# Kernel tuning notes

Measured on AMD Instinct MI355X. Metric: run time of the kernel, lower is better.

The kernel has to match this reference:

```python
import jax, jax.numpy as jnp
import numpy as np

N = 50000      # nodes
E = 800000     # edges
P = 200000     # link pairs
D_IN = 128     # input_dim
F_NUM = 128    # filter_num
OUT = 2        # out_dim
K = 10         # APPNP propagation steps
ALPHA = 0.1    # teleport prob


def setup_inputs() -> dict:
    key = jax.random.key(0)
    ks = jax.random.split(key, 9)
    x = jax.random.normal(ks[0], (N, D_IN), dtype=jnp.float32)
    edge_index = jax.random.randint(ks[1], (2, E), 0, N)
    index = jax.random.randint(ks[2], (P, 2), 0, N)
    s1 = 1.0 / np.sqrt(D_IN)
    s2 = 1.0 / np.sqrt(F_NUM)
    s3 = 1.0 / np.sqrt(2 * F_NUM)
    W1 = jax.random.uniform(ks[3], (F_NUM, D_IN), minval=-s1, maxval=s1)
    b1 = jax.random.uniform(ks[4], (F_NUM,), minval=-s1, maxval=s1)
    W2 = jax.random.uniform(ks[5], (F_NUM, F_NUM), minval=-s2, maxval=s2)
    b2 = jax.random.uniform(ks[6], (F_NUM,), minval=-s2, maxval=s2)
    W3 = jax.random.uniform(ks[7], (OUT, 2 * F_NUM), minval=-s3, maxval=s3)
    b3 = jax.random.uniform(ks[8], (OUT,), minval=-s3, maxval=s3)
    return {"x": x, "edge_index": edge_index, "index": index,
            "W1": W1, "b1": b1, "W2": W2, "b2": b2, "W3": W3, "b3": b3}


def _gcn_norm(edge_index, num_nodes):
    # PyG gcn_norm: add self-loops, sym norm D^{-1/2} (A+I) D^{-1/2}
    src, dst = edge_index[0], edge_index[1]
    loop = jnp.arange(num_nodes, dtype=src.dtype)
    src = jnp.concatenate([src, loop])
    dst = jnp.concatenate([dst, loop])
    deg = jax.ops.segment_sum(jnp.ones_like(src, dtype=jnp.float32), dst,
                              num_segments=num_nodes)
    dinv = jnp.where(deg > 0, jax.lax.rsqrt(deg), 0.0)
    norm = dinv[src] * dinv[dst]  # [E+N]
    return src, dst, norm


def _appnp(x, src, dst, norm, num_nodes):
    # h_{k+1} = (1-alpha) * A_hat h_k + alpha * x0
    def step(h, _):
        agg = jax.ops.segment_sum(norm[:, None] * h[src], dst,
                                  num_segments=num_nodes)
        return (1.0 - ALPHA) * agg + ALPHA * x, None
    h, _ = jax.lax.scan(step, x, None, length=K)
    return h


def reference(x, edge_index, index, W1, b1, W2, b2, W3, b3):
    num_nodes = x.shape[0]
    src, dst, norm = _gcn_norm(edge_index, num_nodes)
    h = x @ W1.T + b1                      # [N, F]
    h = jax.nn.relu(_appnp(h, src, dst, norm, num_nodes))
    h = h @ W2.T + b2                      # [N, F]
    h = jax.nn.relu(_appnp(h, src, dst, norm, num_nodes))
    feat = jnp.concatenate([h[index[:, 0]], h[index[:, 1]]], axis=-1)  # [P, 2F]
    out = feat @ W3.T + b3                 # [P, OUT]
    return jax.nn.log_softmax(out, axis=1)
```

## Files before the change

### kernel.cpp

```cpp
#include <hip/hip_runtime.h>
#include <math.h>

#define NN 50000
#define NE 800000
#define NP 200000
#define NF 128
#define NEDGE_TOT (NE + NN)
#define NBLK 196

typedef __attribute__((ext_vector_type(8))) short short8;
typedef __attribute__((ext_vector_type(4))) float float4v;

__device__ __forceinline__ float bf_lo(unsigned u) { return __uint_as_float(u << 16); }
__device__ __forceinline__ float bf_hi(unsigned u) { return __uint_as_float(u & 0xffff0000u); }
__device__ __forceinline__ unsigned short f2bf(float f) {
    unsigned u = __float_as_uint(f);
    return (unsigned short)((u + 0x7fffu + ((u >> 16) & 1u)) >> 16);
}
__device__ __forceinline__ unsigned pack2bf(float a, float b) {
    return (unsigned)f2bf(a) | ((unsigned)f2bf(b) << 16);
}

__global__ __launch_bounds__(256) void init_cnt_k(int* __restrict__ cnt) {
    int i = blockIdx.x * 256 + threadIdx.x;
    if (i < NN) cnt[i] = 1;
}

__global__ __launch_bounds__(256) void count_k(const int* __restrict__ ei,
                                               int* __restrict__ cnt) {
    int e = blockIdx.x * 256 + threadIdx.x;
    if (e < NE) atomicAdd(&cnt[ei[NE + e]], 1);
}

__global__ __launch_bounds__(256) void scan_reduce_k(const int* __restrict__ cnt,
                                                     int* __restrict__ bsum,
                                                     float* __restrict__ dinv) {
    __shared__ int s[256];
    int t = threadIdx.x;
    int idx = blockIdx.x * 256 + t;
    int v = (idx < NN) ? cnt[idx] : 0;
    if (idx < NN) dinv[idx] = rsqrtf((float)v);
    s[t] = v;
    __syncthreads();
    for (int off = 128; off > 0; off >>= 1) {
        if (t < off) s[t] += s[t + off];
        __syncthreads();
    }
    if (t == 0) bsum[blockIdx.x] = s[0];
}

__global__ __launch_bounds__(256) void scan_bsums_k(const int* __restrict__ bsum,
                                                    int* __restrict__ boff) {
    __shared__ int s[256];
    int t = threadIdx.x;
    int v = (t < NBLK) ? bsum[t] : 0;
    s[t] = v;
    __syncthreads();
    for (int off = 1; off < 256; off <<= 1) {
        int add = (t >= off) ? s[t - off] : 0;
        __syncthreads();
        s[t] += add;
        __syncthreads();
    }
    if (t < NBLK) boff[t] = s[t] - v;
}

__global__ __launch_bounds__(256) void scan_down_k(const int* __restrict__ cnt,
                                                   const int* __restrict__ boff,
                                                   int* __restrict__ row_ptr,
                                                   int* __restrict__ wptr) {
    __shared__ int s[256];
    int t = threadIdx.x;
    int idx = blockIdx.x * 256 + t;
    int v = (idx < NN) ? cnt[idx] : 0;
    s[t] = v;
    __syncthreads();
    for (int off = 1; off < 256; off <<= 1) {
        int add = (t >= off) ? s[t - off] : 0;
        __syncthreads();
        s[t] += add;
        __syncthreads();
    }
    int excl = s[t] - v + boff[blockIdx.x];
    if (idx < NN) {
        row_ptr[idx] = excl;
        wptr[idx] = excl;
        if (idx == NN - 1) row_ptr[NN] = excl + v;
    }
}

__global__ __launch_bounds__(256) void scatter_k(const int* __restrict__ ei,
                                                 const float* __restrict__ dinv,
                                                 int* __restrict__ wptr,
                                                 int* __restrict__ cols,
                                                 float* __restrict__ norms) {
    int e = blockIdx.x * 256 + threadIdx.x;
    if (e >= NEDGE_TOT) return;
    int s, d;
    if (e < NE) { s = ei[e]; d = ei[NE + e]; }
    else        { s = d = e - NE; }
    int pos = atomicAdd(&wptr[d], 1);
    cols[pos]  = s;
    norms[pos] = dinv[s] * dinv[d];
}

__global__ __launch_bounds__(256) void cast_x_k(const float* __restrict__ x,
                                                unsigned short* __restrict__ Xb) {
    int t = blockIdx.x * 256 + threadIdx.x;
    if (t >= NN * 16) return;
    int i = t * 8;
    float4 f0 = *(const float4*)(x + i);
    float4 f1 = *(const float4*)(x + i + 4);
    uint4 q;
    q.x = pack2bf(f0.x, f0.y);
    q.y = pack2bf(f0.z, f0.w);
    q.z = pack2bf(f1.x, f1.y);
    q.w = pack2bf(f1.z, f1.w);
    *(uint4*)(Xb + i) = q;
}

__global__ __launch_bounds__(256) void cast_w_k(const float* __restrict__ W,
                                                unsigned short* __restrict__ Wb) {
    int t = blockIdx.x * 256 + threadIdx.x;
    if (t >= 128 * 128 / 8) return;
    int i = t * 8;
    float4 f0 = *(const float4*)(W + i);
    float4 f1 = *(const float4*)(W + i + 4);
    uint4 q;
    q.x = pack2bf(f0.x, f0.y);
    q.y = pack2bf(f0.z, f0.w);
    q.z = pack2bf(f1.x, f1.y);
    q.w = pack2bf(f1.z, f1.w);
    *(uint4*)(Wb + i) = q;
}

#define GPAD 136
__global__ __launch_bounds__(256) void gemm_mfma_k(const unsigned short* __restrict__ Xb,
                                                   const unsigned short* __restrict__ Wb,
                                                   const float* __restrict__ bias,
                                                   unsigned short* __restrict__ Yb,
                                                   int nrows) {
    __shared__ unsigned short sm[4 * 16 * GPAD];
    int wave = threadIdx.x >> 6, lane = threadIdx.x & 63;
    int rbase = blockIdx.x * 64 + wave * 16;
    if (rbase >= nrows) return;
    int quad = lane >> 4, mn = lane & 15;
    float4v acc[8];
#pragma unroll
    for (int ft = 0; ft < 8; ++ft) acc[ft] = (float4v){0.f, 0.f, 0.f, 0.f};
#pragma unroll
    for (int kb = 0; kb < 128; kb += 32) {
        short8 a = *(const short8*)(Xb + (size_t)(rbase + mn) * NF + kb + quad * 8);
#pragma unroll
        for (int ft = 0; ft < 8; ++ft) {
            short8 b = *(const short8*)(Wb + (size_t)(ft * 16 + mn) * NF + kb + quad * 8);
            acc[ft] = __builtin_amdgcn_mfma_f32_16x16x32_bf16(a, b, acc[ft], 0, 0, 0);
        }
    }
    unsigned short* smw = sm + wave * 16 * GPAD;
#pragma unroll
    for (int ft = 0; ft < 8; ++ft) {
        float bv = bias[ft * 16 + mn];
#pragma unroll
        for (int r = 0; r < 4; ++r)
            smw[(quad * 4 + r) * GPAD + ft * 16 + mn] = f2bf(acc[ft][r] + bv);
    }
    __syncthreads();
#pragma unroll
    for (int t = 0; t < 4; ++t) {
        int rl = t * 4 + quad;
        uint4 q = *(const uint4*)(smw + rl * GPAD + mn * 8);
        *(uint4*)(Yb + (size_t)(rbase + rl) * NF + mn * 8) = q;
    }
}

__global__ __launch_bounds__(256) void appnp_bf16_k(const unsigned short* __restrict__ h,
                                                    const unsigned short* __restrict__ x0,
                                                    unsigned short* __restrict__ out,
                                                    const int* __restrict__ row_ptr,
                                                    const int* __restrict__ cols,
                                                    const float* __restrict__ norms,
                                                    int relu) {
    int wid = (blockIdx.x * 256 + threadIdx.x) >> 6;
    int lane = threadIdx.x & 63;
    if (wid >= NN) return;
    int half = lane >> 5, li = lane & 31;
    int beg = row_ptr[wid], end = row_ptr[wid + 1];
    float a0 = 0.f, a1 = 0.f, a2 = 0.f, a3 = 0.f;
    for (int e = beg; e < end; e += 64) {
        int m = end - e;
        if (m > 64) m = 64;
        int c = 0;
        float w = 0.f;
        if (lane < m) { c = cols[e + lane]; w = norms[e + lane]; }
        int j = 0;
        for (; j + 8 <= m; j += 8) {
#pragma unroll
            for (int p = 0; p < 4; ++p) {
                int src = j + 2 * p + half;
                int cj = __shfl(c, src, 64);
                float wj = __shfl(w, src, 64);
                uint2 q = *((const uint2*)(h + (size_t)cj * NF) + li);
                a0 += wj * bf_lo(q.x);
                a1 += wj * bf_hi(q.x);
                a2 += wj * bf_lo(q.y);
                a3 += wj * bf_hi(q.y);
            }
        }
        for (; j < m; j += 2) {
            int src = j + half;
            int cj = __shfl(c, src, 64);
            float wj = __shfl(w, src, 64);
            uint2 q = *((const uint2*)(h + (size_t)cj * NF) + li);
            a0 += wj * bf_lo(q.x);
            a1 += wj * bf_hi(q.x);
            a2 += wj * bf_lo(q.y);
            a3 += wj * bf_hi(q.y);
        }
    }
    a0 += __shfl_xor(a0, 32, 64);
    a1 += __shfl_xor(a1, 32, 64);
    a2 += __shfl_xor(a2, 32, 64);
    a3 += __shfl_xor(a3, 32, 64);
    if (half == 0) {
        uint2 xq = *((const uint2*)(x0 + (size_t)wid * NF) + li);
        float r0 = 0.9f * a0 + 0.1f * bf_lo(xq.x);
        float r1 = 0.9f * a1 + 0.1f * bf_hi(xq.x);
        float r2 = 0.9f * a2 + 0.1f * bf_lo(xq.y);
        float r3 = 0.9f * a3 + 0.1f * bf_hi(xq.y);
        if (relu) {
            r0 = fmaxf(r0, 0.f); r1 = fmaxf(r1, 0.f);
            r2 = fmaxf(r2, 0.f); r3 = fmaxf(r3, 0.f);
        }
        uint2 oq;
        oq.x = pack2bf(r0, r1);
        oq.y = pack2bf(r2, r3);
        *((uint2*)(out + (size_t)wid * NF) + li) = oq;
    }
}

__global__ __launch_bounds__(256) void pair_k(const unsigned short* __restrict__ h,
                                              const int* __restrict__ index,
                                              const float* __restrict__ W3,
                                              const float* __restrict__ b3,
                                              float* __restrict__ outp) {
    int gw = (blockIdx.x * 256 + threadIdx.x) >> 6;
    int lane = threadIdx.x & 63;
    if (gw >= NP) return;
    int half = lane >> 5, li = lane & 31;
    int u = index[gw * 2], v = index[gw * 2 + 1];
    int node = half ? v : u;
    uint2 q = *((const uint2*)(h + (size_t)node * NF) + li);
    float f0 = bf_lo(q.x), f1 = bf_hi(q.x), f2 = bf_lo(q.y), f3 = bf_hi(q.y);
    int fb = half * 128 + li * 4;
    float4 wa = *(const float4*)(W3 + fb);
    float4 wb = *(const float4*)(W3 + 256 + fb);
    float p0 = f0 * wa.x + f1 * wa.y + f2 * wa.z + f3 * wa.w;
    float p1 = f0 * wb.x + f1 * wb.y + f2 * wb.z + f3 * wb.w;
#pragma unroll
    for (int off = 32; off > 0; off >>= 1) {
        p0 += __shfl_xor(p0, off, 64);
        p1 += __shfl_xor(p1, off, 64);
    }
    if (lane == 0) {
        float s0 = p0 + b3[0], s1 = p1 + b3[1];
        float m = fmaxf(s0, s1);
        float lse = m + logf(expf(s0 - m) + expf(s1 - m));
        *(float2*)(outp + (size_t)gw * 2) = make_float2(s0 - lse, s1 - lse);
    }
}

extern "C" void kernel_launch(void* const* d_in, const int* in_sizes, int n_in,
                              void* d_out, int out_size, void* d_ws, size_t ws_size,
                              hipStream_t stream) {
    const float* x  = (const float*)d_in[0];
    const int* ei   = (const int*)d_in[1];
    const int* idx  = (const int*)d_in[2];
    const float* W1 = (const float*)d_in[3];
    const float* b1 = (const float*)d_in[4];
    const float* W2 = (const float*)d_in[5];
    const float* b2 = (const float*)d_in[6];
    const float* W3 = (const float*)d_in[7];
    const float* b3 = (const float*)d_in[8];
    float* out = (float*)d_out;

    char* ws = (char*)d_ws;
    size_t off = 0;
    auto alloc = [&](size_t bytes) -> void* {
        void* p = ws + off;
        off = (off + bytes + 255) & ~(size_t)255;
        return p;
    };
    int*   cnt     = (int*)  alloc(NN * sizeof(int));
    float* dinv    = (float*)alloc(NN * sizeof(float));
    int*   row_ptr = (int*)  alloc((NN + 1) * sizeof(int));
    int*   wptr    = (int*)  alloc(NN * sizeof(int));
    int*   bsum    = (int*)  alloc(NBLK * sizeof(int));
    int*   boff    = (int*)  alloc(NBLK * sizeof(int));
    int*   cols    = (int*)  alloc(NEDGE_TOT * sizeof(int));
    float* norms   = (float*)alloc(NEDGE_TOT * sizeof(float));
    unsigned short* Xb  = (unsigned short*)alloc((size_t)NN * NF * 2);
    unsigned short* Wb1 = (unsigned short*)alloc(128 * 128 * 2);
    unsigned short* Wb2 = (unsigned short*)alloc(128 * 128 * 2);
    unsigned short* H0  = (unsigned short*)alloc((size_t)NN * NF * 2);
    unsigned short* HA  = (unsigned short*)alloc((size_t)NN * NF * 2);
    unsigned short* HB  = (unsigned short*)alloc((size_t)NN * NF * 2);

    const int gN    = (NN + 255) / 256;
    const int gE    = (NE + 255) / 256;
    const int gET   = (NEDGE_TOT + 255) / 256;
    const int gGemm = (NN + 63) / 64;
    const int gStep = (NN * 64 + 255) / 256;
    const int gPair = (NP * 64 + 255) / 256;

    cast_w_k<<<8, 256, 0, stream>>>(W1, Wb1);
    cast_w_k<<<8, 256, 0, stream>>>(W2, Wb2);
    cast_x_k<<<(NN * 16 + 255) / 256, 256, 0, stream>>>(x, Xb);
    init_cnt_k<<<gN, 256, 0, stream>>>(cnt);
    count_k<<<gE, 256, 0, stream>>>(ei, cnt);
    scan_reduce_k<<<NBLK, 256, 0, stream>>>(cnt, bsum, dinv);
    scan_bsums_k<<<1, 256, 0, stream>>>(bsum, boff);
    scan_down_k<<<NBLK, 256, 0, stream>>>(cnt, boff, row_ptr, wptr);
    scatter_k<<<gET, 256, 0, stream>>>(ei, dinv, wptr, cols, norms);

    gemm_mfma_k<<<gGemm, 256, 0, stream>>>(Xb, Wb1, b1, H0, NN);
    {
        const unsigned short* cur = H0;
        for (int k = 0; k < 10; ++k) {
            unsigned short* dst = (k & 1) ? HB : HA;
            appnp_bf16_k<<<gStep, 256, 0, stream>>>(cur, H0, dst, row_ptr, cols,
                                                    norms, (k == 9) ? 1 : 0);
            cur = dst;
        }
    }
    gemm_mfma_k<<<gGemm, 256, 0, stream>>>(HB, Wb2, b2, H0, NN);
    {
        const unsigned short* cur = H0;
        for (int k = 0; k < 10; ++k) {
            unsigned short* dst = (k & 1) ? HB : HA;
            appnp_bf16_k<<<gStep, 256, 0, stream>>>(cur, H0, dst, row_ptr, cols,
                                                    norms, (k == 9) ? 1 : 0);
            cur = dst;
        }
    }
    pair_k<<<gPair, 256, 0, stream>>>(HB, idx, W3, b3, out);
}
```

Measured before the change: 919.3 us.

## Pack edge records, gather four neighbors per wave, precompute per-node link projections

Edge column and norm are interleaved into one int2 array so each edge needs a single load. The APPNP kernel now splits the wave into four 16-lane groups, each reading a full 256-byte row with uint4 loads. That processes four neighbors per iteration, with a cross-group shuffle reduction at the end. The last propagation step projects each node onto the W3 halves, so the pair kernel reads two float4 per pair instead of two full feature rows. This removes most of the per-pair gather traffic at the cost of more registers and a small change in summation order.

```diff
diff --git a/kernel.cpp b/kernel.cpp
--- a/kernel.cpp
+++ b/kernel.cpp
@@ -92,16 +92,17 @@
 __global__ __launch_bounds__(256) void scatter_k(const int* __restrict__ ei,
                                                  const float* __restrict__ dinv,
                                                  int* __restrict__ wptr,
-                                                 int* __restrict__ cols,
-                                                 float* __restrict__ norms) {
+                                                 int2* __restrict__ rec) {
     int e = blockIdx.x * 256 + threadIdx.x;
     if (e >= NEDGE_TOT) return;
     int s, d;
     if (e < NE) { s = ei[e]; d = ei[NE + e]; }
     else        { s = d = e - NE; }
     int pos = atomicAdd(&wptr[d], 1);
-    cols[pos]  = s;
-    norms[pos] = dinv[s] * dinv[d];
+    int2 r;
+    r.x = s;
+    r.y = __float_as_int(dinv[s] * dinv[d]);
+    rec[pos] = r;
 }
 
 __global__ __launch_bounds__(256) void cast_x_k(const float* __restrict__ x,
@@ -174,100 +175,122 @@
     }
 }
 
-__global__ __launch_bounds__(256) void appnp_bf16_k(const unsigned short* __restrict__ h,
-                                                    const unsigned short* __restrict__ x0,
-                                                    unsigned short* __restrict__ out,
-                                                    const int* __restrict__ row_ptr,
-                                                    const int* __restrict__ cols,
-                                                    const float* __restrict__ norms,
-                                                    int relu) {
+__global__ __launch_bounds__(256) void appnp4_k(const unsigned short* __restrict__ h,
+                                                const unsigned short* __restrict__ x0,
+                                                unsigned short* __restrict__ out,
+                                                const int* __restrict__ row_ptr,
+                                                const int2* __restrict__ rec,
+                                                int relu, int proj,
+                                                const float* __restrict__ W3,
+                                                float4* __restrict__ puv) {
     int wid = (blockIdx.x * 256 + threadIdx.x) >> 6;
     int lane = threadIdx.x & 63;
     if (wid >= NN) return;
-    int half = lane >> 5, li = lane & 31;
+    int g = lane >> 4, li = lane & 15;
     int beg = row_ptr[wid], end = row_ptr[wid + 1];
     float a0 = 0.f, a1 = 0.f, a2 = 0.f, a3 = 0.f;
+    float a4 = 0.f, a5 = 0.f, a6 = 0.f, a7 = 0.f;
     for (int e = beg; e < end; e += 64) {
         int m = end - e;
         if (m > 64) m = 64;
         int c = 0;
         float w = 0.f;
-        if (lane < m) { c = cols[e + lane]; w = norms[e + lane]; }
-        int j = 0;
-        for (; j + 8 <= m; j += 8) {
-#pragma unroll
-            for (int p = 0; p < 4; ++p) {
-                int src = j + 2 * p + half;
-                int cj = __shfl(c, src, 64);
-                float wj = __shfl(w, src, 64);
-                uint2 q = *((const uint2*)(h + (size_t)cj * NF) + li);
+        if (lane < m) { int2 q = rec[e + lane]; c = q.x; w = __int_as_float(q.y); }
+        for (int j = 0; j < m; j += 4) {
+            int src = j + g;
+            int cj = __shfl(c, src, 64);
+            float wj = __shfl(w, src, 64);
+            if (src < m) {
+                uint4 q = *((const uint4*)(h + (size_t)cj * NF) + li);
                 a0 += wj * bf_lo(q.x);
                 a1 += wj * bf_hi(q.x);
                 a2 += wj * bf_lo(q.y);
                 a3 += wj * bf_hi(q.y);
+                a4 += wj * bf_lo(q.z);
+                a5 += wj * bf_hi(q.z);
+                a6 += wj * bf_lo(q.w);
+                a7 += wj * bf_hi(q.w);
             }
         }
-        for (; j < m; j += 2) {
-            int src = j + half;
-            int cj = __shfl(c, src, 64);
-            float wj = __shfl(w, src, 64);
-            uint2 q = *((const uint2*)(h + (size_t)cj * NF) + li);
-            a0 += wj * bf_lo(q.x);
-            a1 += wj * bf_hi(q.x);
-            a2 += wj * bf_lo(q.y);
-            a3 += wj * bf_hi(q.y);
-        }
-    }
-    a0 += __shfl_xor(a0, 32, 64);
-    a1 += __shfl_xor(a1, 32, 64);
-    a2 += __shfl_xor(a2, 32, 64);
-    a3 += __shfl_xor(a3, 32, 64);
-    if (half == 0) {
-        uint2 xq = *((const uint2*)(x0 + (size_t)wid * NF) + li);
+    }
+#pragma unroll
+    for (int off = 16; off < 64; off <<= 1) {
+        a0 += __shfl_xor(a0, off, 64);
+        a1 += __shfl_xor(a1, off, 64);
+        a2 += __shfl_xor(a2, off, 64);
+        a3 += __shfl_xor(a3, off, 64);
+        a4 += __shfl_xor(a4, off, 64);
+        a5 += __shfl_xor(a5, off, 64);
+        a6 += __shfl_xor(a6, off, 64);
+        a7 += __shfl_xor(a7, off, 64);
+    }
+    if (g == 0) {
+        uint4 xq = *((const uint4*)(x0 + (size_t)wid * NF) + li);
         float r0 = 0.9f * a0 + 0.1f * bf_lo(xq.x);
         float r1 = 0.9f * a1 + 0.1f * bf_hi(xq.x);
         float r2 = 0.9f * a2 + 0.1f * bf_lo(xq.y);
         float r3 = 0.9f * a3 + 0.1f * bf_hi(xq.y);
+        float r4 = 0.9f * a4 + 0.1f * bf_lo(xq.z);
+        float r5 = 0.9f * a5 + 0.1f * bf_hi(xq.z);
+        float r6 = 0.9f * a6 + 0.1f * bf_lo(xq.w);
+        float r7 = 0.9f * a7 + 0.1f * bf_hi(xq.w);
         if (relu) {
             r0 = fmaxf(r0, 0.f); r1 = fmaxf(r1, 0.f);
             r2 = fmaxf(r2, 0.f); r3 = fmaxf(r3, 0.f);
-        }
-        uint2 oq;
-        oq.x = pack2bf(r0, r1);
-        oq.y = pack2bf(r2, r3);
-        *((uint2*)(out + (size_t)wid * NF) + li) = oq;
-    }
-}
-
-__global__ __launch_bounds__(256) void pair_k(const unsigned short* __restrict__ h,
-                                              const int* __restrict__ index,
-                                              const float* __restrict__ W3,
-                                              const float* __restrict__ b3,
-                                              float* __restrict__ outp) {
-    int gw = (blockIdx.x * 256 + threadIdx.x) >> 6;
-    int lane = threadIdx.x & 63;
-    if (gw >= NP) return;
-    int half = lane >> 5, li = lane & 31;
-    int u = index[gw * 2], v = index[gw * 2 + 1];
-    int node = half ? v : u;
-    uint2 q = *((const uint2*)(h + (size_t)node * NF) + li);
-    float f0 = bf_lo(q.x), f1 = bf_hi(q.x), f2 = bf_lo(q.y), f3 = bf_hi(q.y);
-    int fb = half * 128 + li * 4;
-    float4 wa = *(const float4*)(W3 + fb);
-    float4 wb = *(const float4*)(W3 + 256 + fb);
-    float p0 = f0 * wa.x + f1 * wa.y + f2 * wa.z + f3 * wa.w;
-    float p1 = f0 * wb.x + f1 * wb.y + f2 * wb.z + f3 * wb.w;
-#pragma unroll
-    for (int off = 32; off > 0; off >>= 1) {
-        p0 += __shfl_xor(p0, off, 64);
-        p1 += __shfl_xor(p1, off, 64);
-    }
-    if (lane == 0) {
-        float s0 = p0 + b3[0], s1 = p1 + b3[1];
-        float m = fmaxf(s0, s1);
-        float lse = m + logf(expf(s0 - m) + expf(s1 - m));
-        *(float2*)(outp + (size_t)gw * 2) = make_float2(s0 - lse, s1 - lse);
-    }
+            r4 = fmaxf(r4, 0.f); r5 = fmaxf(r5, 0.f);
+            r6 = fmaxf(r6, 0.f); r7 = fmaxf(r7, 0.f);
+        }
+        if (!proj) {
+            uint4 oq;
+            oq.x = pack2bf(r0, r1);
+            oq.y = pack2bf(r2, r3);
+            oq.z = pack2bf(r4, r5);
+            oq.w = pack2bf(r6, r7);
+            *((uint4*)(out + (size_t)wid * NF) + li) = oq;
+        } else {
+            int fb = li * 8;
+            float4 wu0a = *(const float4*)(W3 + fb);
+            float4 wu0b = *(const float4*)(W3 + fb + 4);
+            float4 wv0a = *(const float4*)(W3 + 128 + fb);
+            float4 wv0b = *(const float4*)(W3 + 128 + fb + 4);
+            float4 wu1a = *(const float4*)(W3 + 256 + fb);
+            float4 wu1b = *(const float4*)(W3 + 256 + fb + 4);
+            float4 wv1a = *(const float4*)(W3 + 384 + fb);
+            float4 wv1b = *(const float4*)(W3 + 384 + fb + 4);
+            float du0 = r0 * wu0a.x + r1 * wu0a.y + r2 * wu0a.z + r3 * wu0a.w
+                      + r4 * wu0b.x + r5 * wu0b.y + r6 * wu0b.z + r7 * wu0b.w;
+            float du1 = r0 * wu1a.x + r1 * wu1a.y + r2 * wu1a.z + r3 * wu1a.w
+                      + r4 * wu1b.x + r5 * wu1b.y + r6 * wu1b.z + r7 * wu1b.w;
+            float dv0 = r0 * wv0a.x + r1 * wv0a.y + r2 * wv0a.z + r3 * wv0a.w
+                      + r4 * wv0b.x + r5 * wv0b.y + r6 * wv0b.z + r7 * wv0b.w;
+            float dv1 = r0 * wv1a.x + r1 * wv1a.y + r2 * wv1a.z + r3 * wv1a.w
+                      + r4 * wv1b.x + r5 * wv1b.y + r6 * wv1b.z + r7 * wv1b.w;
+#pragma unroll
+            for (int off = 1; off < 16; off <<= 1) {
+                du0 += __shfl_xor(du0, off, 64);
+                du1 += __shfl_xor(du1, off, 64);
+                dv0 += __shfl_xor(dv0, off, 64);
+                dv1 += __shfl_xor(dv1, off, 64);
+            }
+            if (li == 0) puv[wid] = make_float4(du0, du1, dv0, dv1);
+        }
+    }
+}
+
+__global__ __launch_bounds__(256) void pair2_k(const float4* __restrict__ puv,
+                                               const int2* __restrict__ index,
+                                               const float* __restrict__ b3,
+                                               float* __restrict__ outp) {
+    int p = blockIdx.x * 256 + threadIdx.x;
+    if (p >= NP) return;
+    int2 uv = index[p];
+    float4 a = puv[uv.x];
+    float4 b = puv[uv.y];
+    float s0 = a.x + b.z + b3[0];
+    float s1 = a.y + b.w + b3[1];
+    float m = fmaxf(s0, s1);
+    float lse = m + logf(expf(s0 - m) + expf(s1 - m));
+    *(float2*)(outp + (size_t)p * 2) = make_float2(s0 - lse, s1 - lse);
 }
 
 extern "C" void kernel_launch(void* const* d_in, const int* in_sizes, int n_in,
@@ -297,8 +320,8 @@
     int*   wptr    = (int*)  alloc(NN * sizeof(int));
     int*   bsum    = (int*)  alloc(NBLK * sizeof(int));
     int*   boff    = (int*)  alloc(NBLK * sizeof(int));
-    int*   cols    = (int*)  alloc(NEDGE_TOT * sizeof(int));
-    float* norms   = (float*)alloc(NEDGE_TOT * sizeof(float));
+    int2*  rec     = (int2*) alloc((size_t)NEDGE_TOT * sizeof(int2));
+    float4* puv    = (float4*)alloc((size_t)NN * sizeof(float4));
     unsigned short* Xb  = (unsigned short*)alloc((size_t)NN * NF * 2);
     unsigned short* Wb1 = (unsigned short*)alloc(128 * 128 * 2);
     unsigned short* Wb2 = (unsigned short*)alloc(128 * 128 * 2);
@@ -311,7 +334,7 @@
     const int gET   = (NEDGE_TOT + 255) / 256;
     const int gGemm = (NN + 63) / 64;
     const int gStep = (NN * 64 + 255) / 256;
-    const int gPair = (NP * 64 + 255) / 256;
+    const int gPair = (NP + 255) / 256;
 
     cast_w_k<<<8, 256, 0, stream>>>(W1, Wb1);
     cast_w_k<<<8, 256, 0, stream>>>(W2, Wb2);
@@ -321,15 +344,15 @@
     scan_reduce_k<<<NBLK, 256, 0, stream>>>(cnt, bsum, dinv);
     scan_bsums_k<<<1, 256, 0, stream>>>(bsum, boff);
     scan_down_k<<<NBLK, 256, 0, stream>>>(cnt, boff, row_ptr, wptr);
-    scatter_k<<<gET, 256, 0, stream>>>(ei, dinv, wptr, cols, norms);
+    scatter_k<<<gET, 256, 0, stream>>>(ei, dinv, wptr, rec);
 
     gemm_mfma_k<<<gGemm, 256, 0, stream>>>(Xb, Wb1, b1, H0, NN);
     {
         const unsigned short* cur = H0;
         for (int k = 0; k < 10; ++k) {
             unsigned short* dst = (k & 1) ? HB : HA;
-            appnp_bf16_k<<<gStep, 256, 0, stream>>>(cur, H0, dst, row_ptr, cols,
-                                                    norms, (k == 9) ? 1 : 0);
+            appnp4_k<<<gStep, 256, 0, stream>>>(cur, H0, dst, row_ptr, rec,
+                                                (k == 9) ? 1 : 0, 0, W3, puv);
             cur = dst;
         }
     }
@@ -338,10 +361,11 @@
         const unsigned short* cur = H0;
         for (int k = 0; k < 10; ++k) {
             unsigned short* dst = (k & 1) ? HB : HA;
-            appnp_bf16_k<<<gStep, 256, 0, stream>>>(cur, H0, dst, row_ptr, cols,
-                                                    norms, (k == 9) ? 1 : 0);
+            appnp4_k<<<gStep, 256, 0, stream>>>(cur, H0, dst, row_ptr, rec,
+                                                (k == 9) ? 1 : 0,
+                                                (k == 9) ? 1 : 0, W3, puv);
             cur = dst;
         }
     }
-    pair_k<<<gPair, 256, 0, stream>>>(HB, idx, W3, b3, out);
-}
+    pair2_k<<<gPair, 256, 0, stream>>>(puv, (const int2*)idx, b3, out);
+}
```

Result: no change. 909.7 us (-1.0%).

## Factor GCN norm into pre-scaled features, fuse casts and final projection

Applied to the files above, without the earlier changes.

Stores the propagated features pre-multiplied by dinv, so each APPNP step is an unweighted gather-sum plus one per-node scale, and the per-edge norms array is removed. The fp32 input cast is folded into the first GEMM. The final W3 projection is pushed into the last propagation step as per-node scalars, so the pair kernel reads 16 bytes per node instead of full feature rows. A zeroed padding row replaces masked edge lanes, which allows four independent gathers per iteration. The cost is extra bf16 rounding of the scaled features and more workspace buffers.

```diff
diff --git a/kernel.cpp b/kernel.cpp
--- a/kernel.cpp
+++ b/kernel.cpp
@@ -90,33 +90,23 @@
 }
 
 __global__ __launch_bounds__(256) void scatter_k(const int* __restrict__ ei,
-                                                 const float* __restrict__ dinv,
                                                  int* __restrict__ wptr,
-                                                 int* __restrict__ cols,
-                                                 float* __restrict__ norms) {
+                                                 int* __restrict__ cols) {
     int e = blockIdx.x * 256 + threadIdx.x;
     if (e >= NEDGE_TOT) return;
     int s, d;
     if (e < NE) { s = ei[e]; d = ei[NE + e]; }
     else        { s = d = e - NE; }
     int pos = atomicAdd(&wptr[d], 1);
-    cols[pos]  = s;
-    norms[pos] = dinv[s] * dinv[d];
-}
-
-__global__ __launch_bounds__(256) void cast_x_k(const float* __restrict__ x,
-                                                unsigned short* __restrict__ Xb) {
-    int t = blockIdx.x * 256 + threadIdx.x;
-    if (t >= NN * 16) return;
-    int i = t * 8;
-    float4 f0 = *(const float4*)(x + i);
-    float4 f1 = *(const float4*)(x + i + 4);
-    uint4 q;
-    q.x = pack2bf(f0.x, f0.y);
-    q.y = pack2bf(f0.z, f0.w);
-    q.z = pack2bf(f1.x, f1.y);
-    q.w = pack2bf(f1.z, f1.w);
-    *(uint4*)(Xb + i) = q;
+    cols[pos] = s;
+}
+
+__global__ __launch_bounds__(256) void zero_k(unsigned short* Ys1, unsigned short* Ys2,
+                                              unsigned short* HA, unsigned short* HB) {
+    int t = threadIdx.x;
+    unsigned short* bufs[4] = {Ys1, Ys2, HA, HB};
+    unsigned short* b = bufs[t >> 6];
+    ((unsigned*)(b + (size_t)NN * NF))[t & 63] = 0u;
 }
 
 __global__ __launch_bounds__(256) void cast_w_k(const float* __restrict__ W,
@@ -135,10 +125,13 @@
 }
 
 #define GPAD 136
-__global__ __launch_bounds__(256) void gemm_mfma_k(const unsigned short* __restrict__ Xb,
+template <bool F32IN>
+__global__ __launch_bounds__(256) void gemm_mfma_k(const void* __restrict__ Xv,
                                                    const unsigned short* __restrict__ Wb,
                                                    const float* __restrict__ bias,
-                                                   unsigned short* __restrict__ Yb,
+                                                   const float* __restrict__ dinv,
+                                                   unsigned short* __restrict__ Yu,
+                                                   unsigned short* __restrict__ Ys,
                                                    int nrows) {
     __shared__ unsigned short sm[4 * 16 * GPAD];
     int wave = threadIdx.x >> 6, lane = threadIdx.x & 63;
@@ -150,7 +143,19 @@
     for (int ft = 0; ft < 8; ++ft) acc[ft] = (float4v){0.f, 0.f, 0.f, 0.f};
 #pragma unroll
     for (int kb = 0; kb < 128; kb += 32) {
-        short8 a = *(const short8*)(Xb + (size_t)(rbase + mn) * NF + kb + quad * 8);
+        short8 a;
+        if (F32IN) {
+            const float* X = (const float*)Xv;
+            float4 f0 = *(const float4*)(X + (size_t)(rbase + mn) * NF + kb + quad * 8);
+            float4 f1 = *(const float4*)(X + (size_t)(rbase + mn) * NF + kb + quad * 8 + 4);
+            a[0] = (short)f2bf(f0.x); a[1] = (short)f2bf(f0.y);
+            a[2] = (short)f2bf(f0.z); a[3] = (short)f2bf(f0.w);
+            a[4] = (short)f2bf(f1.x); a[5] = (short)f2bf(f1.y);
+            a[6] = (short)f2bf(f1.z); a[7] = (short)f2bf(f1.w);
+        } else {
+            const unsigned short* X = (const unsigned short*)Xv;
+            a = *(const short8*)(X + (size_t)(rbase + mn) * NF + kb + quad * 8);
+        }
 #pragma unroll
         for (int ft = 0; ft < 8; ++ft) {
             short8 b = *(const short8*)(Wb + (size_t)(ft * 16 + mn) * NF + kb + quad * 8);
@@ -169,18 +174,28 @@
 #pragma unroll
     for (int t = 0; t < 4; ++t) {
         int rl = t * 4 + quad;
+        int row = rbase + rl;
         uint4 q = *(const uint4*)(smw + rl * GPAD + mn * 8);
-        *(uint4*)(Yb + (size_t)(rbase + rl) * NF + mn * 8) = q;
-    }
-}
-
-__global__ __launch_bounds__(256) void appnp_bf16_k(const unsigned short* __restrict__ h,
-                                                    const unsigned short* __restrict__ x0,
-                                                    unsigned short* __restrict__ out,
-                                                    const int* __restrict__ row_ptr,
-                                                    const int* __restrict__ cols,
-                                                    const float* __restrict__ norms,
-                                                    int relu) {
+        *(uint4*)(Yu + (size_t)row * NF + mn * 8) = q;
+        float g = dinv[row];
+        uint4 qs;
+        qs.x = pack2bf(g * bf_lo(q.x), g * bf_hi(q.x));
+        qs.y = pack2bf(g * bf_lo(q.y), g * bf_hi(q.y));
+        qs.z = pack2bf(g * bf_lo(q.z), g * bf_hi(q.z));
+        qs.w = pack2bf(g * bf_lo(q.w), g * bf_hi(q.w));
+        *(uint4*)(Ys + (size_t)row * NF + mn * 8) = qs;
+    }
+}
+
+__global__ __launch_bounds__(256) void appnp_s_k(const unsigned short* __restrict__ hs,
+                                                 const unsigned short* __restrict__ x0,
+                                                 const float* __restrict__ dinv,
+                                                 unsigned short* __restrict__ out,
+                                                 const int* __restrict__ row_ptr,
+                                                 const int* __restrict__ cols,
+                                                 int mode,
+                                                 const float* __restrict__ W3,
+                                                 float4* __restrict__ puv) {
     int wid = (blockIdx.x * 256 + threadIdx.x) >> 6;
     int lane = threadIdx.x & 63;
     if (wid >= NN) return;
@@ -190,32 +205,29 @@
     for (int e = beg; e < end; e += 64) {
         int m = end - e;
         if (m > 64) m = 64;
-        int c = 0;
-        float w = 0.f;
-        if (lane < m) { c = cols[e + lane]; w = norms[e + lane]; }
+        int c = (lane < m) ? cols[e + lane] : NN;
         int j = 0;
         for (; j + 8 <= m; j += 8) {
-#pragma unroll
-            for (int p = 0; p < 4; ++p) {
-                int src = j + 2 * p + half;
-                int cj = __shfl(c, src, 64);
-                float wj = __shfl(w, src, 64);
-                uint2 q = *((const uint2*)(h + (size_t)cj * NF) + li);
-                a0 += wj * bf_lo(q.x);
-                a1 += wj * bf_hi(q.x);
-                a2 += wj * bf_lo(q.y);
-                a3 += wj * bf_hi(q.y);
-            }
+            int c0 = __shfl(c, j + half, 64);
+            int c1 = __shfl(c, j + 2 + half, 64);
+            int c2 = __shfl(c, j + 4 + half, 64);
+            int c3 = __shfl(c, j + 6 + half, 64);
+            uint2 q0 = *((const uint2*)(hs + (size_t)c0 * NF) + li);
+            uint2 q1 = *((const uint2*)(hs + (size_t)c1 * NF) + li);
+            uint2 q2 = *((const uint2*)(hs + (size_t)c2 * NF) + li);
+            uint2 q3 = *((const uint2*)(hs + (size_t)c3 * NF) + li);
+            a0 += (bf_lo(q0.x) + bf_lo(q1.x)) + (bf_lo(q2.x) + bf_lo(q3.x));
+            a1 += (bf_hi(q0.x) + bf_hi(q1.x)) + (bf_hi(q2.x) + bf_hi(q3.x));
+            a2 += (bf_lo(q0.y) + bf_lo(q1.y)) + (bf_lo(q2.y) + bf_lo(q3.y));
+            a3 += (bf_hi(q0.y) + bf_hi(q1.y)) + (bf_hi(q2.y) + bf_hi(q3.y));
         }
         for (; j < m; j += 2) {
-            int src = j + half;
-            int cj = __shfl(c, src, 64);
-            float wj = __shfl(w, src, 64);
-            uint2 q = *((const uint2*)(h + (size_t)cj * NF) + li);
-            a0 += wj * bf_lo(q.x);
-            a1 += wj * bf_hi(q.x);
-            a2 += wj * bf_lo(q.y);
-            a3 += wj * bf_hi(q.y);
+            int cj = __shfl(c, j + half, 64);
+            uint2 q = *((const uint2*)(hs + (size_t)cj * NF) + li);
+            a0 += bf_lo(q.x);
+            a1 += bf_hi(q.x);
+            a2 += bf_lo(q.y);
+            a3 += bf_hi(q.y);
         }
     }
     a0 += __shfl_xor(a0, 32, 64);
@@ -223,51 +235,63 @@
     a2 += __shfl_xor(a2, 32, 64);
     a3 += __shfl_xor(a3, 32, 64);
     if (half == 0) {
+        float g = dinv[wid];
+        float s9 = 0.9f * g;
         uint2 xq = *((const uint2*)(x0 + (size_t)wid * NF) + li);
-        float r0 = 0.9f * a0 + 0.1f * bf_lo(xq.x);
-        float r1 = 0.9f * a1 + 0.1f * bf_hi(xq.x);
-        float r2 = 0.9f * a2 + 0.1f * bf_lo(xq.y);
-        float r3 = 0.9f * a3 + 0.1f * bf_hi(xq.y);
-        if (relu) {
-            r0 = fmaxf(r0, 0.f); r1 = fmaxf(r1, 0.f);
-            r2 = fmaxf(r2, 0.f); r3 = fmaxf(r3, 0.f);
-        }
-        uint2 oq;
-        oq.x = pack2bf(r0, r1);
-        oq.y = pack2bf(r2, r3);
-        *((uint2*)(out + (size_t)wid * NF) + li) = oq;
-    }
-}
-
-__global__ __launch_bounds__(256) void pair_k(const unsigned short* __restrict__ h,
-                                              const int* __restrict__ index,
-                                              const float* __restrict__ W3,
-                                              const float* __restrict__ b3,
-                                              float* __restrict__ outp) {
-    int gw = (blockIdx.x * 256 + threadIdx.x) >> 6;
-    int lane = threadIdx.x & 63;
-    if (gw >= NP) return;
-    int half = lane >> 5, li = lane & 31;
-    int u = index[gw * 2], v = index[gw * 2 + 1];
-    int node = half ? v : u;
-    uint2 q = *((const uint2*)(h + (size_t)node * NF) + li);
-    float f0 = bf_lo(q.x), f1 = bf_hi(q.x), f2 = bf_lo(q.y), f3 = bf_hi(q.y);
-    int fb = half * 128 + li * 4;
-    float4 wa = *(const float4*)(W3 + fb);
-    float4 wb = *(const float4*)(W3 + 256 + fb);
-    float p0 = f0 * wa.x + f1 * wa.y + f2 * wa.z + f3 * wa.w;
-    float p1 = f0 * wb.x + f1 * wb.y + f2 * wb.z + f3 * wb.w;
-#pragma unroll
-    for (int off = 32; off > 0; off >>= 1) {
-        p0 += __shfl_xor(p0, off, 64);
-        p1 += __shfl_xor(p1, off, 64);
-    }
-    if (lane == 0) {
-        float s0 = p0 + b3[0], s1 = p1 + b3[1];
-        float m = fmaxf(s0, s1);
-        float lse = m + logf(expf(s0 - m) + expf(s1 - m));
-        *(float2*)(outp + (size_t)gw * 2) = make_float2(s0 - lse, s1 - lse);
-    }
+        float h0 = s9 * a0 + 0.1f * bf_lo(xq.x);
+        float h1 = s9 * a1 + 0.1f * bf_hi(xq.x);
+        float h2 = s9 * a2 + 0.1f * bf_lo(xq.y);
+        float h3 = s9 * a3 + 0.1f * bf_hi(xq.y);
+        if (mode == 0) {
+            uint2 oq;
+            oq.x = pack2bf(g * h0, g * h1);
+            oq.y = pack2bf(g * h2, g * h3);
+            *((uint2*)(out + (size_t)wid * NF) + li) = oq;
+        } else {
+            h0 = fmaxf(h0, 0.f); h1 = fmaxf(h1, 0.f);
+            h2 = fmaxf(h2, 0.f); h3 = fmaxf(h3, 0.f);
+            if (mode == 1) {
+                uint2 oq;
+                oq.x = pack2bf(h0, h1);
+                oq.y = pack2bf(h2, h3);
+                *((uint2*)(out + (size_t)wid * NF) + li) = oq;
+            } else {
+                int fb = li * 4;
+                float4 wu0 = *(const float4*)(W3 + fb);
+                float4 wv0 = *(const float4*)(W3 + 128 + fb);
+                float4 wu1 = *(const float4*)(W3 + 256 + fb);
+                float4 wv1 = *(const float4*)(W3 + 384 + fb);
+                float du0 = h0 * wu0.x + h1 * wu0.y + h2 * wu0.z + h3 * wu0.w;
+                float du1 = h0 * wu1.x + h1 * wu1.y + h2 * wu1.z + h3 * wu1.w;
+                float dv0 = h0 * wv0.x + h1 * wv0.y + h2 * wv0.z + h3 * wv0.w;
+                float dv1 = h0 * wv1.x + h1 * wv1.y + h2 * wv1.z + h3 * wv1.w;
+#pragma unroll
+                for (int off = 1; off < 32; off <<= 1) {
+                    du0 += __shfl_xor(du0, off, 64);
+                    du1 += __shfl_xor(du1, off, 64);
+                    dv0 += __shfl_xor(dv0, off, 64);
+                    dv1 += __shfl_xor(dv1, off, 64);
+                }
+                if (li == 0) puv[wid] = make_float4(du0, du1, dv0, dv1);
+            }
+        }
+    }
+}
+
+__global__ __launch_bounds__(256) void pair2_k(const float4* __restrict__ puv,
+                                               const int2* __restrict__ index,
+                                               const float* __restrict__ b3,
+                                               float* __restrict__ outp) {
+    int p = blockIdx.x * 256 + threadIdx.x;
+    if (p >= NP) return;
+    int2 uv = index[p];
+    float4 a = puv[uv.x];
+    float4 b = puv[uv.y];
+    float s0 = a.x + b.z + b3[0];
+    float s1 = a.y + b.w + b3[1];
+    float m = fmaxf(s0, s1);
+    float lse = m + logf(expf(s0 - m) + expf(s1 - m));
+    *(float2*)(outp + (size_t)p * 2) = make_float2(s0 - lse, s1 - lse);
 }
 
 extern "C" void kernel_launch(void* const* d_in, const int* in_sizes, int n_in,
@@ -291,57 +315,61 @@
         off = (off + bytes + 255) & ~(size_t)255;
         return p;
     };
+    const size_t HROWS = (size_t)(NN + 1) * NF;
     int*   cnt     = (int*)  alloc(NN * sizeof(int));
     float* dinv    = (float*)alloc(NN * sizeof(float));
     int*   row_ptr = (int*)  alloc((NN + 1) * sizeof(int));
     int*   wptr    = (int*)  alloc(NN * sizeof(int));
     int*   bsum    = (int*)  alloc(NBLK * sizeof(int));
     int*   boff    = (int*)  alloc(NBLK * sizeof(int));
-    int*   cols    = (int*)  alloc(NEDGE_TOT * sizeof(int));
-    float* norms   = (float*)alloc(NEDGE_TOT * sizeof(float));
-    unsigned short* Xb  = (unsigned short*)alloc((size_t)NN * NF * 2);
+    int*   cols    = (int*)  alloc((size_t)NEDGE_TOT * sizeof(int));
+    float4* puv    = (float4*)alloc((size_t)NN * sizeof(float4));
     unsigned short* Wb1 = (unsigned short*)alloc(128 * 128 * 2);
     unsigned short* Wb2 = (unsigned short*)alloc(128 * 128 * 2);
-    unsigned short* H0  = (unsigned short*)alloc((size_t)NN * NF * 2);
-    unsigned short* HA  = (unsigned short*)alloc((size_t)NN * NF * 2);
-    unsigned short* HB  = (unsigned short*)alloc((size_t)NN * NF * 2);
+    unsigned short* Yu1 = (unsigned short*)alloc(HROWS * 2);
+    unsigned short* Ys1 = (unsigned short*)alloc(HROWS * 2);
+    unsigned short* Yu2 = (unsigned short*)alloc(HROWS * 2);
+    unsigned short* Ys2 = (unsigned short*)alloc(HROWS * 2);
+    unsigned short* HA  = (unsigned short*)alloc(HROWS * 2);
+    unsigned short* HB  = (unsigned short*)alloc(HROWS * 2);
+    unsigned short* Hrelu = (unsigned short*)alloc((size_t)NN * NF * 2);
 
     const int gN    = (NN + 255) / 256;
     const int gE    = (NE + 255) / 256;
     const int gET   = (NEDGE_TOT + 255) / 256;
     const int gGemm = (NN + 63) / 64;
     const int gStep = (NN * 64 + 255) / 256;
-    const int gPair = (NP * 64 + 255) / 256;
+    const int gPair = (NP + 255) / 256;
 
     cast_w_k<<<8, 256, 0, stream>>>(W1, Wb1);
     cast_w_k<<<8, 256, 0, stream>>>(W2, Wb2);
-    cast_x_k<<<(NN * 16 + 255) / 256, 256, 0, stream>>>(x, Xb);
     init_cnt_k<<<gN, 256, 0, stream>>>(cnt);
     count_k<<<gE, 256, 0, stream>>>(ei, cnt);
     scan_reduce_k<<<NBLK, 256, 0, stream>>>(cnt, bsum, dinv);
     scan_bsums_k<<<1, 256, 0, stream>>>(bsum, boff);
     scan_down_k<<<NBLK, 256, 0, stream>>>(cnt, boff, row_ptr, wptr);
-    scatter_k<<<gET, 256, 0, stream>>>(ei, dinv, wptr, cols, norms);
-
-    gemm_mfma_k<<<gGemm, 256, 0, stream>>>(Xb, Wb1, b1, H0, NN);
+    scatter_k<<<gET, 256, 0, stream>>>(ei, wptr, cols);
+    zero_k<<<1, 256, 0, stream>>>(Ys1, Ys2, HA, HB);
+
+    gemm_mfma_k<true><<<gGemm, 256, 0, stream>>>(x, Wb1, b1, dinv, Yu1, Ys1, NN);
     {
-        const unsigned short* cur = H0;
+        const unsigned short* cur = Ys1;
+        for (int k = 0; k < 10; ++k) {
+            unsigned short* dst = (k == 9) ? Hrelu : ((k & 1) ? HB : HA);
+            appnp_s_k<<<gStep, 256, 0, stream>>>(cur, Yu1, dinv, dst, row_ptr,
+                                                 cols, (k == 9) ? 1 : 0, W3, puv);
+            cur = dst;
+        }
+    }
+    gemm_mfma_k<false><<<gGemm, 256, 0, stream>>>(Hrelu, Wb2, b2, dinv, Yu2, Ys2, NN);
+    {
+        const unsigned short* cur = Ys2;
         for (int k = 0; k < 10; ++k) {
             unsigned short* dst = (k & 1) ? HB : HA;
-            appnp_bf16_k<<<gStep, 256, 0, stream>>>(cur, H0, dst, row_ptr, cols,
-                                                    norms, (k == 9) ? 1 : 0);
+            appnp_s_k<<<gStep, 256, 0, stream>>>(cur, Yu2, dinv, dst, row_ptr,
+                                                 cols, (k == 9) ? 2 : 0, W3, puv);
             cur = dst;
         }
     }
-    gemm_mfma_k<<<gGemm, 256, 0, stream>>>(HB, Wb2, b2, H0, NN);
-    {
-        const unsigned short* cur = H0;
-        for (int k = 0; k < 10; ++k) {
-            unsigned short* dst = (k & 1) ? HB : HA;
-            appnp_bf16_k<<<gStep, 256, 0, stream>>>(cur, H0, dst, row_ptr, cols,
-                                                    norms, (k == 9) ? 1 : 0);
-            cur = dst;
-        }
-    }
-    pair_k<<<gPair, 256, 0, stream>>>(HB, idx, W3, b3, out);
-}
+    pair2_k<<<gPair, 256, 0, stream>>>(puv, (const int2*)idx, b3, out);
+}
```

Result: faster. 883.3 us (-3.9%).
